# Performance work log

Measured on AMD Instinct MI355X. Metric: run time of the kernel, lower is better.

## Reference

```python
import jax, jax.numpy as jnp
import numpy as np
from jax import lax

# dims
N, CIN, COUT, CI, T, V = 128, 64, 64, 16, 128, 25
SS, ST = 3, 2  # num_subset_S, num_subset_T
BN_EPS = 1e-5
LRELU = 0.1


def _bn(x, p):
    # x: [N,C,T,V]; p: [4,C] = (gamma, beta, running_mean, running_var), eval-mode BN
    g, b, m, v = p
    inv = g / jnp.sqrt(v + BN_EPS)
    return (x - m[:, None, None]) * inv[:, None, None] + b[:, None, None]


def _c1x1(x, w, b):
    # 1x1 Conv2d: x [N,C,T,V], w [O,C], b [O]
    return jnp.einsum('nctv,oc->notv', x, w) + b[None, :, None, None]


def _lrelu(x):
    return jnp.where(x >= 0, x, LRELU * x)


def _bn_params(c):
    return jnp.stack([jnp.ones(c, jnp.float32), jnp.zeros(c, jnp.float32),
                      jnp.zeros(c, jnp.float32), jnp.ones(c, jnp.float32)])


def setup_inputs() -> dict:
    key = jax.random.key(0)
    ks = jax.random.split(key, 12)
    d = {}
    d['x'] = jax.random.normal(ks[0], (N, CIN, T, V), jnp.float32)
    # spatial attention projections
    d['w_in_s'] = jax.random.normal(ks[1], (2 * SS * CI, CIN), jnp.float32) * 0.1
    d['b_in_s'] = jnp.zeros((2 * SS * CI,), jnp.float32)
    d['alphas'] = jnp.ones((1, SS, 1, 1), jnp.float32)
    d['att0s'] = jnp.ones((1, SS, V, V), jnp.float32) / V
    d['w_out_s'] = jax.random.normal(ks[2], (COUT, SS * CIN), jnp.float32) * 0.05
    d['b_out_s'] = jnp.zeros((COUT,), jnp.float32)
    d['bn_out_s'] = _bn_params(COUT)
    d['w_ff_s'] = jax.random.normal(ks[3], (COUT, COUT), jnp.float32) * 0.1
    d['b_ff_s'] = jnp.zeros((COUT,), jnp.float32)
    d['bn_ff_s'] = _bn_params(COUT)
    # temporal attention projections (directed)
    d['w_in_t'] = jax.random.normal(ks[4], (4 * ST * CI, COUT), jnp.float32) * 0.1
    d['b_in_t'] = jnp.zeros((4 * ST * CI,), jnp.float32)
    d['alphat_f'] = jnp.ones((1, ST, 1, 1), jnp.float32)
    d['alphat_b'] = jnp.ones((1, ST, 1, 1), jnp.float32)
    d['w_out_t'] = jax.random.normal(ks[5], (COUT, 2 * ST * COUT), jnp.float32) * 0.05
    d['b_out_t'] = jnp.zeros((COUT,), jnp.float32)
    d['bn_out_t'] = _bn_params(COUT)
    d['w_ff_t'] = jax.random.normal(ks[6], (COUT, COUT), jnp.float32) * 0.1
    d['b_ff_t'] = jnp.zeros((COUT,), jnp.float32)
    d['bn_ff_t'] = _bn_params(COUT)
    # TCN extension (7x1 temporal conv)
    d['w_tcn'] = jax.random.normal(ks[7], (COUT, COUT, 7, 1), jnp.float32) * 0.03
    d['b_tcn'] = jnp.zeros((COUT,), jnp.float32)
    d['bn_tcn'] = _bn_params(COUT)
    return d


def _forward(x, w_in_s, b_in_s, alphas, att0s, w_out_s, b_out_s, bn_out_s,
             w_ff_s, b_ff_s, bn_ff_s, w_in_t, b_in_t, alphat_f, alphat_b,
             w_out_t, b_out_t, bn_out_t, w_ff_t, b_ff_t, bn_ff_t,
             w_tcn, b_tcn, bn_tcn):
    n, c, t, v = x.shape
    # ---- spatial attention ----
    qk = _c1x1(x, w_in_s, b_in_s).reshape(n, 2 * SS, CI, t, v)
    q, k = qk[:, :SS], qk[:, SS:]
    # atts buffer is zeros; attention = tanh(QK/(ci*T))*alpha + attention0s
    attn = jnp.tanh(jnp.einsum('nsctu,nsctv->nsuv', q, k) / (CI * t)) * alphas + att0s
    y = jnp.einsum('nctu,nsuv->nsctv', x, attn).reshape(n, SS * c, t, v)
    y = _bn(_c1x1(y, w_out_s, b_out_s), bn_out_s)
    y = _lrelu(x + y)            # downs1 = identity
    y2 = _bn(_c1x1(y, w_ff_s, b_ff_s), bn_ff_s)
    y = _lrelu(x + y2)           # downs2 = identity
    # ---- temporal attention (directed) ----
    qk = _c1x1(y, w_in_t, b_in_t).reshape(n, 4 * ST, CI, t, v)
    q_f, q_b = qk[:, :ST], qk[:, ST:2 * ST]
    k_f, k_b = qk[:, 2 * ST:3 * ST], qk[:, 3 * ST:]
    bmask = jnp.triu(jnp.ones((t, t), x.dtype))
    fmask = bmask.T
    a_b = jnp.tanh(jnp.einsum('nsctv,nscqv->nstq', q_b, k_b) / (CI * v)) * alphat_b * bmask
    a_f = jnp.tanh(jnp.einsum('nsctv,nscqv->nstq', q_f, k_f) / (CI * v)) * alphat_f * fmask
    z_f = jnp.einsum('nctv,nstq->nscqv', y, a_f).reshape(n, ST * COUT, t, v)
    z_b = jnp.einsum('nctv,nstq->nscqv', y, a_b).reshape(n, ST * COUT, t, v)
    z = jnp.concatenate([z_f, z_b], axis=1)
    z = _bn(_c1x1(z, w_out_t, b_out_t), bn_out_t)
    z = _lrelu(y + z)            # downt1 = identity
    z2 = _bn(_c1x1(z, w_ff_t, b_ff_t), bn_ff_t)
    z = _lrelu(y + z2)           # downt2 = identity
    # ---- TCN extension: residual 7x1 temporal conv, downt3 = identity ----
    tcn = lax.conv_general_dilated(z, w_tcn, (1, 1), ((3, 3), (0, 0)),
                                   dimension_numbers=('NCHW', 'OIHW', 'NCHW'))
    tcn = _bn(tcn + b_tcn[None, :, None, None], bn_tcn)
    z = _lrelu(z + tcn)
    return z


def reference(x, w_in_s, b_in_s, alphas, att0s, w_out_s, b_out_s, bn_out_s,
              w_ff_s, b_ff_s, bn_ff_s, w_in_t, b_in_t, alphat_f, alphat_b,
              w_out_t, b_out_t, bn_out_t, w_ff_t, b_ff_t, bn_ff_t,
              w_tcn, b_tcn, bn_tcn):
    return _forward(x, w_in_s, b_in_s, alphas, att0s, w_out_s, b_out_s, bn_out_s,
                    w_ff_s, b_ff_s, bn_ff_s, w_in_t, b_in_t, alphat_f, alphat_b,
                    w_out_t, b_out_t, bn_out_t, w_ff_t, b_ff_t, bn_ff_t,
                    w_tcn, b_tcn, bn_tcn)
```

## Files before the change

kernel.cpp:

```cpp
#include <hip/hip_runtime.h>
#include <math.h>

#define NN   128
#define TTc  128
#define VVc  25
#define TV   3200
#define BN_EPS 1e-5f

typedef __attribute__((ext_vector_type(8))) short bf8;
typedef __attribute__((ext_vector_type(4))) short s4;
typedef __attribute__((ext_vector_type(4))) float f4;

#define MFMA(a,b,c) __builtin_amdgcn_mfma_f32_16x16x32_bf16(a,b,c,0,0,0)

__device__ __forceinline__ float lrelu(float a){ return a>=0.f ? a : 0.1f*a; }
__device__ __forceinline__ short f2bs(float f){
    union{float f; unsigned u;} x; x.f = f;
    unsigned r = x.u + 0x7FFF + ((x.u>>16)&1);
    return (short)(r>>16);
}
__device__ __forceinline__ float b2f(short s){
    union{unsigned u; float f;} x; x.u = ((unsigned)(unsigned short)s)<<16; return x.f;
}
__device__ __forceinline__ s4 packf4(float a,float b,float c,float d){
    s4 r; r.x=f2bs(a); r.y=f2bs(b); r.z=f2bs(c); r.w=f2bs(d); return r;
}


__global__ __launch_bounds__(256) void k_prep(
    const float* __restrict__ w_in_s, const float* __restrict__ w_out_s,
    const float* __restrict__ w_ff_s, const float* __restrict__ w_in_t,
    const float* __restrict__ w_out_t, const float* __restrict__ w_ff_t,
    const float* __restrict__ w_tcn, short* __restrict__ wb)
{
    const int total = 51200 + 64*448;
    for (int i = blockIdx.x*256 + threadIdx.x; i < total; i += gridDim.x*256) {
        float v;
        if      (i < 6144)  v = w_in_s[i];
        else if (i < 18432) v = w_out_s[i-6144];
        else if (i < 22528) v = w_ff_s[i-18432];
        else if (i < 30720) v = w_in_t[i-22528];
        else if (i < 47104) v = w_out_t[i-30720];
        else if (i < 51200) v = w_ff_t[i-47104];
        else { int j=i-51200; int o=j/448; int r=j%448; int dt=r>>6; int c=r&63;
               v = w_tcn[(o*64+c)*7 + dt]; }
        wb[i] = f2bs(v);
    }
}

__global__ __launch_bounds__(256) void k_x2b(const float* __restrict__ x, short* __restrict__ XB)
{
    const int n = blockIdx.x >> 4, tc = blockIdx.x & 15, t0 = tc*8;
    const int tid = threadIdx.x;
    __shared__ float xs[64][203];
    const float* xb = x + (size_t)n*204800 + t0*25;
    for (int i = tid; i < 64*200; i += 256) { int c=i/200, p=i%200; xs[c][p] = xb[(size_t)c*3200 + p]; }
    __syncthreads();
    short* ob = XB + (size_t)n*204800 + t0*25*64;
    for (int i = tid; i < 200*16; i += 256) {
        const int p = i>>4, c0 = (i&15)<<2;
        *(s4*)&ob[p*64 + c0] = packf4(xs[c0][p], xs[c0+1][p], xs[c0+2][p], xs[c0+3][p]);
    }
}

__global__ __launch_bounds__(256) void k_attn_s(
    const short* __restrict__ XB, const short* __restrict__ wb,
    const float* __restrict__ b_in_s, const float* __restrict__ alphas,
    const float* __restrict__ att0s, short* __restrict__ attnB)
{
    const int n = blockIdx.x / 3, s = blockIdx.x % 3;
    const int tid = threadIdx.x, w = tid>>6, lane = tid&63, lr = lane&15, lq = lane>>4;
    __shared__ short ys[208][72];
    __shared__ short qkl[208][40];
    __shared__ short wsl[32][72];
    __shared__ float bl[32];

    for (int i = tid; i < 32*8; i += 256) {
        const int cl = i>>3, seg = i&7;
        const int row = (cl < 16) ? (s*16 + cl) : (48 + s*16 + (cl-16));
        *(bf8*)&wsl[cl][seg*8] = *(const bf8*)&wb[row*64 + seg*8];
    }
    if (tid < 32) {
        const int row = (tid < 16) ? (s*16 + tid) : (48 + s*16 + (tid-16));
        bl[tid] = b_in_s[row];
    }

    const int mt = w>>1, sn = w&1;
    f4 acc = {0.f,0.f,0.f,0.f};

    for (int ch = 0; ch < 16; ++ch) {
        __syncthreads();
        for (int i = tid; i < 208*8; i += 256) {
            const int row = i>>3, seg = i&7;
            bf8 val = {0,0,0,0,0,0,0,0};
            if (row < 200)
                val = *(const bf8*)&XB[((size_t)n*3200 + ch*200 + row)*64 + seg*8];
            *(bf8*)&ys[row][seg*8] = val;
        }
        __syncthreads();
        for (int nn = 0; nn < 4; ++nn) {
            const int nt2 = w + nn*4;
            if (nt2 >= 13) break;
            const bf8 b0 = *(const bf8*)&ys[nt2*16+lr][lq*8];
            const bf8 b1 = *(const bf8*)&ys[nt2*16+lr][32+lq*8];
            for (int mt2 = 0; mt2 < 2; ++mt2) {
                f4 pa = {0.f,0.f,0.f,0.f};
                const bf8 a0 = *(const bf8*)&wsl[mt2*16+lr][lq*8];
                const bf8 a1 = *(const bf8*)&wsl[mt2*16+lr][32+lq*8];
                pa = MFMA(a0,b0,pa); pa = MFMA(a1,b1,pa);
                const int px = nt2*16+lr, c0 = mt2*16+lq*4;
                *(s4*)&qkl[px][c0] =
                    packf4(pa.x+bl[c0], pa.y+bl[c0+1], pa.z+bl[c0+2], pa.w+bl[c0+3]);
            }
        }
        __syncthreads();
        for (int ks = 0; ks < 4; ++ks) {
            const int tl = ks*2 + (lq>>1);
            const bf8 af = *(const bf8*)&qkl[tl*25 + mt*16+lr][(lq&1)*8];
            const bf8 bf = *(const bf8*)&qkl[tl*25 + sn*16+lr][16 + (lq&1)*8];
            acc = MFMA(af, bf, acc);
        }
    }
    const float alpha = alphas[s];
    const int v = sn*16 + lr, u0 = mt*16 + lq*4;
    float r[4];
    #pragma unroll
    for (int j = 0; j < 4; ++j) {
        const int u = u0 + j;
        const float a = (j==0)?acc.x:((j==1)?acc.y:((j==2)?acc.z:acc.w));
        r[j] = (u < 25 && v < 25)
             ? tanhf(a*(1.f/2048.f))*alpha + att0s[s*625 + u*25 + v] : 0.f;
    }
    *(s4*)&attnB[(size_t)n*3072 + v*96 + s*32 + u0] = packf4(r[0],r[1],r[2],r[3]);
}

__global__ __launch_bounds__(256) void k_spatial(
    const short* __restrict__ XB, const short* __restrict__ attnB, const short* __restrict__ wb,
    const float* __restrict__ b_out, const float* __restrict__ bn_out,
    const float* __restrict__ b_ff,  const float* __restrict__ bn_ff,
    short* __restrict__ Y)
{
    const int n = blockIdx.x >> 5, tc = blockIdx.x & 31, t0 = tc*4;
    const int tid = threadIdx.x;
    const int w = tid>>6, lane = tid&63, lr = lane&15, lq = lane>>4;
    __shared__ short xs[4][32][72];
    __shared__ short wlo[64][200];
    __shared__ short wlf[64][72];
    __shared__ short ab[32][104];
    __shared__ short gsT[4][64][104];
    __shared__ short y1[4][32][72];
    __shared__ float sc1s[64], sh1s[64], sc2s[64], sh2s[64];

    for (int i = tid; i < 4*32*8; i += 256) {
        const int row = i>>3, seg = i&7, tl = row>>5, uv = row&31;
        bf8 val = {0,0,0,0,0,0,0,0};
        if (uv < 25) val = *(const bf8*)&XB[((size_t)n*3200 + (t0+tl)*25 + uv)*64 + seg*8];
        *(bf8*)&xs[tl][uv][seg*8] = val;
    }
    for (int i = tid; i < 64*24; i += 256) {
        const int o = i/24, seg = i%24;
        *(bf8*)&wlo[o][seg*8] = *(const bf8*)&wb[6144 + o*192 + seg*8];
    }
    for (int i = tid; i < 64*8; i += 256) {
        const int o = i>>3, seg = i&7;
        *(bf8*)&wlf[o][seg*8] = *(const bf8*)&wb[18432 + o*64 + seg*8];
    }
    for (int i = tid; i < 32*12; i += 256) {
        const int v = i/12, seg = i%12;
        *(bf8*)&ab[v][seg*8] = *(const bf8*)&attnB[(size_t)n*3072 + v*96 + seg*8];
    }
    if (tid < 64) {
        float g=bn_out[tid], bb=bn_out[64+tid], m=bn_out[128+tid], vv=bn_out[192+tid];
        float inv = g*rsqrtf(vv+BN_EPS);
        sc1s[tid]=inv; sh1s[tid]=(b_out[tid]-m)*inv+bb;
        g=bn_ff[tid]; bb=bn_ff[64+tid]; m=bn_ff[128+tid]; vv=bn_ff[192+tid];
        inv = g*rsqrtf(vv+BN_EPS);
        sc2s[tid]=inv; sh2s[tid]=(b_ff[tid]-m)*inv+bb;
    }
    __syncthreads();

    const int t = t0 + w;
    for (int s = 0; s < 3; ++s) {
        for (int mt = 0; mt < 2; ++mt) {
            const bf8 a0 = *(const bf8*)&xs[w][mt*16+lr][lq*8];
            const bf8 a1 = *(const bf8*)&xs[w][mt*16+lr][32+lq*8];
            for (int nt = 0; nt < 4; ++nt) {
                f4 acc = {0.f,0.f,0.f,0.f};
                const bf8 b0 = *(const bf8*)&wlo[nt*16+lr][s*64 + lq*8];
                const bf8 b1 = *(const bf8*)&wlo[nt*16+lr][s*64 + 32 + lq*8];
                acc = MFMA(a0,b0,acc); acc = MFMA(a1,b1,acc);
                const int o = nt*16+lr, u0 = mt*16+lq*4;
                *(s4*)&gsT[w][o][s*32+u0] = packf4(acc.x,acc.y,acc.z,acc.w);
            }
        }
    }
    for (int mt = 0; mt < 4; ++mt) {
        const bf8 a0 = *(const bf8*)&gsT[w][mt*16+lr][lq*8];
        const bf8 a1 = *(const bf8*)&gsT[w][mt*16+lr][32+lq*8];
        const bf8 a2 = *(const bf8*)&gsT[w][mt*16+lr][64+lq*8];
        for (int nt = 0; nt < 2; ++nt) {
            f4 acc = {0.f,0.f,0.f,0.f};
            const bf8 b0 = *(const bf8*)&ab[nt*16+lr][lq*8];
            const bf8 b1 = *(const bf8*)&ab[nt*16+lr][32+lq*8];
            const bf8 b2 = *(const bf8*)&ab[nt*16+lr][64+lq*8];
            acc = MFMA(a0,b0,acc); acc = MFMA(a1,b1,acc); acc = MFMA(a2,b2,acc);
            const int v = nt*16+lr, o0 = mt*16+lq*4;
            const s4 xr = *(const s4*)&xs[w][v][o0];
            const float r0 = lrelu(acc.x*sc1s[o0  ]+sh1s[o0  ]+b2f(xr.x));
            const float r1 = lrelu(acc.y*sc1s[o0+1]+sh1s[o0+1]+b2f(xr.y));
            const float r2 = lrelu(acc.z*sc1s[o0+2]+sh1s[o0+2]+b2f(xr.z));
            const float r3 = lrelu(acc.w*sc1s[o0+3]+sh1s[o0+3]+b2f(xr.w));
            *(s4*)&y1[w][v][o0] = packf4(r0,r1,r2,r3);
        }
    }
    for (int mt = 0; mt < 4; ++mt) {
        const bf8 a0 = *(const bf8*)&wlf[mt*16+lr][lq*8];
        const bf8 a1 = *(const bf8*)&wlf[mt*16+lr][32+lq*8];
        for (int nt = 0; nt < 2; ++nt) {
            f4 acc = {0.f,0.f,0.f,0.f};
            const bf8 b0 = *(const bf8*)&y1[w][nt*16+lr][lq*8];
            const bf8 b1 = *(const bf8*)&y1[w][nt*16+lr][32+lq*8];
            acc = MFMA(a0,b0,acc); acc = MFMA(a1,b1,acc);
            const int v = nt*16+lr, o0 = mt*16+lq*4;
            if (v < 25) {
                const s4 xr = *(const s4*)&xs[w][v][o0];
                const float r0 = lrelu(acc.x*sc2s[o0  ]+sh2s[o0  ]+b2f(xr.x));
                const float r1 = lrelu(acc.y*sc2s[o0+1]+sh2s[o0+1]+b2f(xr.y));
                const float r2 = lrelu(acc.z*sc2s[o0+2]+sh2s[o0+2]+b2f(xr.z));
                const float r3 = lrelu(acc.w*sc2s[o0+3]+sh2s[o0+3]+b2f(xr.w));
                *(s4*)&Y[((size_t)n*3200 + t*25 + v)*64 + o0] = packf4(r0,r1,r2,r3);
            }
        }
    }
}

__global__ __launch_bounds__(256) void k_qkt(
    const short* __restrict__ Y, const short* __restrict__ wb,
    const float* __restrict__ b_in_t, short* __restrict__ qkt)
{
    const int n = blockIdx.x >> 5, tc = blockIdx.x & 31, t0 = tc*4;
    const int tid = threadIdx.x;
    const int w = tid>>6, lane = tid&63, lr = lane&15, lq = lane>>4;
    __shared__ short ys[4][32][72];
    __shared__ short wi[128][72];
    for (int i = tid; i < 4*32*8; i += 256) {
        const int row = i>>3, seg = i&7, tl = row>>5, v = row&31;
        bf8 val = {0,0,0,0,0,0,0,0};
        if (v < 25) val = *(const bf8*)&Y[((size_t)n*3200 + (t0+tl)*25 + v)*64 + seg*8];
        *(bf8*)&ys[tl][v][seg*8] = val;
    }
    for (int i = tid; i < 128*8; i += 256) {
        const int o = i>>3, seg = i&7;
        *(bf8*)&wi[o][seg*8] = *(const bf8*)&wb[22528 + o*64 + seg*8];
    }
    __syncthreads();
    for (int mi = 0; mi < 2; ++mi) {
        const int mt = w*2+mi, tl = mt>>1, vh = mt&1;
        const bf8 a0 = *(const bf8*)&ys[tl][vh*16+lr][lq*8];
        const bf8 a1 = *(const bf8*)&ys[tl][vh*16+lr][32+lq*8];
        for (int nt = 0; nt < 8; ++nt) {
            f4 acc = {0.f,0.f,0.f,0.f};
            const bf8 b0 = *(const bf8*)&wi[nt*16+lr][lq*8];
            const bf8 b1 = *(const bf8*)&wi[nt*16+lr][32+lq*8];
            acc = MFMA(a0,b0,acc); acc = MFMA(a1,b1,acc);
            const int oc = nt*16+lr, v0 = vh*16+lq*4, t = t0+tl;
            const float bias = b_in_t[oc];
            const size_t base = (size_t)n*409600 + (size_t)t*3200 + oc*25 + v0;
            if (v0 < 24)
                *(s4*)&qkt[base] = packf4(acc.x+bias, acc.y+bias, acc.z+bias, acc.w+bias);
            else if (v0 == 24)
                qkt[base] = f2bs(acc.x+bias);
        }
    }
}

__global__ __launch_bounds__(256) void k_score_t(
    const short* __restrict__ qkt, const float* __restrict__ alphat_f,
    const float* __restrict__ alphat_b, short* __restrict__ aT)
{
    const int n = blockIdx.x >> 2, ds = blockIdx.x & 3, dir = ds>>1, s = ds&1;
    const int qoff = dir*32 + s*16, koff = 64 + dir*32 + s*16;
    const float alpha = dir ? alphat_b[s] : alphat_f[s];
    const int tid = threadIdx.x, w = tid>>6, lane = tid&63, lr = lane&15, lq = lane>>4;
    const short* qb = qkt + (size_t)n*409600;
    short* ao = aT + (size_t)(n*4+ds)*16384;
    const bf8 zf = {0,0,0,0,0,0,0,0};
    for (int ni = 0; ni < 2; ++ni) {
        const int nt = w*2+ni;
        for (int mt = 0; mt < 8; ++mt) {
            const int q = nt*16+lr, t0r = mt*16+lq*4;
            const bool skip = (dir==0) ? (mt < nt) : (mt > nt);
            if (skip) { s4 z = {0,0,0,0}; *(s4*)&ao[q*128 + t0r] = z; continue; }
            f4 acc = {0.f,0.f,0.f,0.f};
            for (int ks = 0; ks < 13; ++ks) {
                bf8 af, bf;
                if (ks==12 && lq>=2) { af = zf; bf = zf; }
                else {
                    af = *(const bf8*)&qb[(size_t)(mt*16+lr)*3200 + qoff*25 + ks*32 + lq*8];
                    bf = *(const bf8*)&qb[(size_t)(nt*16+lr)*3200 + koff*25 + ks*32 + lq*8];
                }
                acc = MFMA(af, bf, acc);
            }
            float r[4];
            #pragma unroll
            for (int j = 0; j < 4; ++j) {
                const int tt = t0r + j;
                const bool ok = (dir==0) ? (tt >= q) : (tt <= q);
                const float a = (j==0)?acc.x:((j==1)?acc.y:((j==2)?acc.z:acc.w));
                r[j] = ok ? tanhf(a*(1.f/400.f))*alpha : 0.f;
            }
            *(s4*)&ao[q*128 + t0r] = packf4(r[0],r[1],r[2],r[3]);
        }
    }
}

__global__ __launch_bounds__(256, 3) void k_tagg(
    const short* __restrict__ Y, const short* __restrict__ wb,
    const short* __restrict__ aT, short* __restrict__ U)
{
    const int n = blockIdx.x / 25, v = blockIdx.x % 25;
    const int tid = threadIdx.x, w = tid>>6, lane = tid&63, lr = lane&15, lq = lane>>4;
    __shared__ short ys[128][72];
    __shared__ short pt[2][64][136];

    for (int i = tid; i < 128*8; i += 256) {
        const int t = i>>3, seg = i&7;
        *(bf8*)&ys[t][seg*8] = *(const bf8*)&Y[((size_t)n*3200 + t*25 + v)*64 + seg*8];
    }
    bf8 wr[4][2];
    #pragma unroll
    for (int ds = 0; ds < 4; ++ds) {
        wr[ds][0] = *(const bf8*)&wb[30720 + (w*16+lr)*256 + ds*64 + lq*8];
        wr[ds][1] = *(const bf8*)&wb[30720 + (w*16+lr)*256 + ds*64 + 32 + lq*8];
    }

    f4 acc[2][4];
    #pragma unroll
    for (int mi = 0; mi < 2; ++mi)
        #pragma unroll
        for (int nt = 0; nt < 4; ++nt) { acc[mi][nt].x=0.f; acc[mi][nt].y=0.f; acc[mi][nt].z=0.f; acc[mi][nt].w=0.f; }

    __syncthreads();

    #pragma unroll
    for (int ds = 0; ds < 4; ++ds) {
        const int dir = ds>>1, buf = ds&1;
        bf8 ar[2][4];
        #pragma unroll
        for (int mi = 0; mi < 2; ++mi) {
            const int qt = 2*w + mi;
            #pragma unroll
            for (int ks = 0; ks < 4; ++ks) {
                const bool skip = (dir==0) ? (ks*32+31 < qt*16) : (ks*32 > qt*16+15);
                if (!skip)
                    ar[mi][ks] = *(const bf8*)&aT[(size_t)(n*4+ds)*16384
                                                  + (qt*16+lr)*128 + ks*32 + lq*8];
            }
        }
        {
            const bf8 b0 = wr[ds][0], b1 = wr[ds][1];
            #pragma unroll
            for (int tt = 0; tt < 8; ++tt) {
                f4 p = {0.f,0.f,0.f,0.f};
                const bf8 a0 = *(const bf8*)&ys[tt*16+lr][lq*8];
                const bf8 a1 = *(const bf8*)&ys[tt*16+lr][32+lq*8];
                p = MFMA(a0,b0,p); p = MFMA(a1,b1,p);
                *(s4*)&pt[buf][w*16+lr][tt*16+lq*4] = packf4(p.x,p.y,p.z,p.w);
            }
        }
        __syncthreads();
        #pragma unroll
        for (int ks = 0; ks < 4; ++ks) {
            const bool skip0 = (dir==0) ? (ks*32+31 < (2*w)*16)   : (ks*32 > (2*w)*16+15);
            const bool skip1 = (dir==0) ? (ks*32+31 < (2*w+1)*16) : (ks*32 > (2*w+1)*16+15);
            if (skip0 && skip1) continue;
            bf8 bfr[4];
            #pragma unroll
            for (int nt = 0; nt < 4; ++nt)
                bfr[nt] = *(const bf8*)&pt[buf][nt*16+lr][ks*32+lq*8];
            if (!skip0) {
                #pragma unroll
                for (int nt = 0; nt < 4; ++nt)
                    acc[0][nt] = MFMA(ar[0][ks], bfr[nt], acc[0][nt]);
            }
            if (!skip1) {
                #pragma unroll
                for (int nt = 0; nt < 4; ++nt)
                    acc[1][nt] = MFMA(ar[1][ks], bfr[nt], acc[1][nt]);
            }
        }
    }
    #pragma unroll
    for (int mi = 0; mi < 2; ++mi) {
        #pragma unroll
        for (int j = 0; j < 4; ++j) {
            const int q = (2*w+mi)*16 + lq*4 + j;
            short* ub = &U[((size_t)(n*128+q)*25 + v)*64 + lr];
            ub[0]  = f2bs(acc[mi][0][j]);
            ub[16] = f2bs(acc[mi][1][j]);
            ub[32] = f2bs(acc[mi][2][j]);
            ub[48] = f2bs(acc[mi][3][j]);
        }
    }
}

__global__ __launch_bounds__(256) void k_temporal(
    const short* __restrict__ U, short* __restrict__ Y, const short* __restrict__ wb,
    const float* __restrict__ b_out, const float* __restrict__ bn_out,
    const float* __restrict__ b_ff,  const float* __restrict__ bn_ff)
{
    const int n = blockIdx.x >> 5, qc = blockIdx.x & 31, q0 = qc*4;
    const int tid = threadIdx.x, w = tid>>6, lane = tid&63, lr = lane&15, lq = lane>>4;
    __shared__ short zs[112][72];
    __shared__ short z1[112][72];
    __shared__ short zout[112][72];
    __shared__ short wf[64][72];
    __shared__ float sc1s[64], sh1s[64], sc2s[64], sh2s[64];
    if (tid < 64) {
        float g=bn_out[tid], bb=bn_out[64+tid], m=bn_out[128+tid], vv=bn_out[192+tid];
        float inv = g*rsqrtf(vv+BN_EPS);
        sc1s[tid]=inv; sh1s[tid]=(b_out[tid]-m)*inv+bb;
        g=bn_ff[tid]; bb=bn_ff[64+tid]; m=bn_ff[128+tid]; vv=bn_ff[192+tid];
        inv = g*rsqrtf(vv+BN_EPS);
        sc2s[tid]=inv; sh2s[tid]=(b_ff[tid]-m)*inv+bb;
    }
    for (int i = tid; i < 64*8; i += 256) {
        const int o = i>>3, seg = i&7;
        *(bf8*)&wf[o][seg*8] = *(const bf8*)&wb[47104 + o*64 + seg*8];
    }
    __syncthreads();
    for (int i = tid; i < 112*8; i += 256) {
        const int row = i>>3, seg = i&7;
        bf8 yv = {0,0,0,0,0,0,0,0}, zv = yv;
        if (row < 100) {
            const int q = q0 + row/25, v = row%25;
            yv = *(const bf8*)&Y[((size_t)n*3200 + q*25 + v)*64 + seg*8];
            const bf8 uv = *(const bf8*)&U[((size_t)(n*128+q)*25 + v)*64 + seg*8];
            #pragma unroll
            for (int j = 0; j < 8; ++j) {
                const int o = seg*8+j;
                zv[j] = f2bs(lrelu(b2f(yv[j]) + b2f(uv[j])*sc1s[o] + sh1s[o]));
            }
        }
        *(bf8*)&zs[row][seg*8] = yv;
        *(bf8*)&z1[row][seg*8] = zv;
    }
    __syncthreads();
    const bf8 a0 = *(const bf8*)&wf[w*16+lr][lq*8];
    const bf8 a1 = *(const bf8*)&wf[w*16+lr][32+lq*8];
    for (int nt = 0; nt < 7; ++nt) {
        f4 acc = {0.f,0.f,0.f,0.f};
        const bf8 b0 = *(const bf8*)&z1[nt*16+lr][lq*8];
        const bf8 b1 = *(const bf8*)&z1[nt*16+lr][32+lq*8];
        acc = MFMA(a0,b0,acc); acc = MFMA(a1,b1,acc);
        const int px = nt*16+lr, o0 = w*16+lq*4;
        const s4 yr = *(const s4*)&zs[px][o0];
        const float r0 = lrelu(acc.x*sc2s[o0  ]+sh2s[o0  ]+b2f(yr.x));
        const float r1 = lrelu(acc.y*sc2s[o0+1]+sh2s[o0+1]+b2f(yr.y));
        const float r2 = lrelu(acc.z*sc2s[o0+2]+sh2s[o0+2]+b2f(yr.z));
        const float r3 = lrelu(acc.w*sc2s[o0+3]+sh2s[o0+3]+b2f(yr.w));
        *(s4*)&zout[px][o0] = packf4(r0,r1,r2,r3);
    }
    __syncthreads();
    for (int i = tid; i < 100*8; i += 256) {
        const int row = i>>3, seg = i&7;
        *(bf8*)&Y[((size_t)n*3200 + q0*25 + row)*64 + seg*8] = *(const bf8*)&zout[row][seg*8];
    }
}

__global__ __launch_bounds__(256, 2) void k_tcn(
    const short* __restrict__ Y, const short* __restrict__ wb,
    const float* __restrict__ b, const float* __restrict__ bn,
    float* __restrict__ out)
{
    const int n = blockIdx.x >> 5, tc = (blockIdx.x >> 1) & 15, oh = blockIdx.x & 1;
    const int t0 = tc*8;
    const int tid = threadIdx.x, w = tid>>6, lane = tid&63, lr = lane&15, lq = lane>>4;
    __shared__ short zs[352][72];
    __shared__ float scs[32], shs[32];

    bf8 af[2][14];
    #pragma unroll
    for (int mt = 0; mt < 2; ++mt)
        #pragma unroll
        for (int st = 0; st < 14; ++st)
            af[mt][st] = *(const bf8*)&wb[51200 + (oh*32 + mt*16 + lr)*448 + st*32 + lq*8];

    if (tid < 32) {
        const int o = oh*32 + tid;
        const float g=bn[o], bb=bn[64+o], m=bn[128+o], vv=bn[192+o];
        const float inv = g*rsqrtf(vv+BN_EPS);
        scs[tid]=inv; shs[tid]=(b[o]-m)*inv+bb;
    }
    for (int i = tid; i < 352*8; i += 256) {
        const int row = i>>3, seg = i&7;
        bf8 val = {0,0,0,0,0,0,0,0};
        if (row < 350) {
            const int tlp = row/25, v = row%25, t = t0 - 3 + tlp;
            if (t >= 0 && t < 128)
                val = *(const bf8*)&Y[((size_t)n*3200 + t*25 + v)*64 + seg*8];
        }
        *(bf8*)&zs[row][seg*8] = val;
    }
    __syncthreads();
    for (int nn = 0; nn < 4; ++nn) {
        const int nt = w + nn*4;
        if (nt >= 13) break;
        bf8 bfr[14];
        #pragma unroll
        for (int st = 0; st < 14; ++st)
            bfr[st] = *(const bf8*)&zs[nt*16 + lr + (st>>1)*25][(st&1)*32 + lq*8];
        f4 ac[2][4];
        #pragma unroll
        for (int m2 = 0; m2 < 2; ++m2)
            #pragma unroll
            for (int j = 0; j < 4; ++j) { ac[m2][j].x=0.f; ac[m2][j].y=0.f; ac[m2][j].z=0.f; ac[m2][j].w=0.f; }
        #pragma unroll
        for (int st = 0; st < 14; ++st) {
            ac[0][st&3] = MFMA(af[0][st], bfr[st], ac[0][st&3]);
            ac[1][st&3] = MFMA(af[1][st], bfr[st], ac[1][st&3]);
        }
        const int px = nt*16+lr;
        if (px < 200) {
            #pragma unroll
            for (int mt = 0; mt < 2; ++mt) {
                const float ax = ac[mt][0].x+ac[mt][1].x+ac[mt][2].x+ac[mt][3].x;
                const float ay = ac[mt][0].y+ac[mt][1].y+ac[mt][2].y+ac[mt][3].y;
                const float az = ac[mt][0].z+ac[mt][1].z+ac[mt][2].z+ac[mt][3].z;
                const float aw = ac[mt][0].w+ac[mt][1].w+ac[mt][2].w+ac[mt][3].w;
                const int o0l = mt*16+lq*4;
                const s4 zr = *(const s4*)&zs[px+75][oh*32+o0l];
                float* ob = out + (size_t)n*204800 + (size_t)(oh*32+o0l)*3200 + t0*25 + px;
                ob[0]    = lrelu(ax*scs[o0l  ]+shs[o0l  ]+b2f(zr.x));
                ob[3200] = lrelu(ay*scs[o0l+1]+shs[o0l+1]+b2f(zr.y));
                ob[6400] = lrelu(az*scs[o0l+2]+shs[o0l+2]+b2f(zr.z));
                ob[9600] = lrelu(aw*scs[o0l+3]+shs[o0l+3]+b2f(zr.w));
            }
        }
    }
}

extern "C" void kernel_launch(void* const* d_in, const int* in_sizes, int n_in,
                              void* d_out, int out_size, void* d_ws, size_t ws_size,
                              hipStream_t stream) {
    const float* x        = (const float*)d_in[0];
    const float* w_in_s   = (const float*)d_in[1];
    const float* b_in_s   = (const float*)d_in[2];
    const float* alphas   = (const float*)d_in[3];
    const float* att0s    = (const float*)d_in[4];
    const float* w_out_s  = (const float*)d_in[5];
    const float* b_out_s  = (const float*)d_in[6];
    const float* bn_out_s = (const float*)d_in[7];
    const float* w_ff_s   = (const float*)d_in[8];
    const float* b_ff_s   = (const float*)d_in[9];
    const float* bn_ff_s  = (const float*)d_in[10];
    const float* w_in_t   = (const float*)d_in[11];
    const float* b_in_t   = (const float*)d_in[12];
    const float* alphat_f = (const float*)d_in[13];
    const float* alphat_b = (const float*)d_in[14];
    const float* w_out_t  = (const float*)d_in[15];
    const float* b_out_t  = (const float*)d_in[16];
    const float* bn_out_t = (const float*)d_in[17];
    const float* w_ff_t   = (const float*)d_in[18];
    const float* b_ff_t   = (const float*)d_in[19];
    const float* bn_ff_t  = (const float*)d_in[20];
    const float* w_tcn    = (const float*)d_in[21];
    const float* b_tcn    = (const float*)d_in[22];
    const float* bn_tcn   = (const float*)d_in[23];
    float* out = (float*)d_out;
    char* ws = (char*)d_ws;

    short* wb    = (short*)(ws + 0);
    short* attnB = (short*)(ws + 4102144);
    short* Y     = (short*)(ws + 4888576);
    short* aT    = (short*)(ws + 57317376);
    short* XB    = (short*)(ws + 74094592);
    short* QKT   = (short*)(ws + 74094592);
    short* U     = (short*)(ws + 74094592 + 52428800);

    k_prep<<<64, 256, 0, stream>>>(w_in_s, w_out_s, w_ff_s, w_in_t, w_out_t, w_ff_t, w_tcn, wb);
    k_x2b<<<2048, 256, 0, stream>>>(x, XB);
    k_attn_s<<<NN * 3, 256, 0, stream>>>(XB, wb, b_in_s, alphas, att0s, attnB);
    k_spatial<<<4096, 256, 0, stream>>>(XB, attnB, wb, b_out_s, bn_out_s, b_ff_s, bn_ff_s, Y);
    k_qkt<<<4096, 256, 0, stream>>>(Y, wb, b_in_t, QKT);
    k_score_t<<<512, 256, 0, stream>>>(QKT, alphat_f, alphat_b, aT);
    k_tagg<<<NN * 25, 256, 0, stream>>>(Y, wb, aT, U);
    k_temporal<<<4096, 256, 0, stream>>>(U, Y, wb, b_out_t, bn_out_t, b_ff_t, bn_ff_t);
    k_tcn<<<4096, 256, 0, stream>>>(Y, wb, b_tcn, bn_tcn, out);
}
```

Before: 714.7 us.

## Keep spatial-kernel weights and attention fragments in registers, shrink LDS use

Rewrites k_spatial so the out-projection, feed-forward weights and attention operands are loaded straight from global memory into register fragments instead of being staged in shared memory. The per-subset intermediate now goes into a smaller LDS buffer, with the attention MFMA accumulated per subset. This cuts LDS footprint and staging work, and launch_bounds(256,2) is requested to raise occupancy. The cost is more register pressure and repeated global (cache) loads of the weights by every wave.

```diff
diff --git a/kernel.cpp b/kernel.cpp
--- a/kernel.cpp
+++ b/kernel.cpp
@@ -134,7 +134,7 @@
     *(s4*)&attnB[(size_t)n*3072 + v*96 + s*32 + u0] = packf4(r[0],r[1],r[2],r[3]);
 }
 
-__global__ __launch_bounds__(256) void k_spatial(
+__global__ __launch_bounds__(256, 2) void k_spatial(
     const short* __restrict__ XB, const short* __restrict__ attnB, const short* __restrict__ wb,
     const float* __restrict__ b_out, const float* __restrict__ bn_out,
     const float* __restrict__ b_ff,  const float* __restrict__ bn_ff,
@@ -144,30 +144,28 @@
     const int tid = threadIdx.x;
     const int w = tid>>6, lane = tid&63, lr = lane&15, lq = lane>>4;
     __shared__ short xs[4][32][72];
-    __shared__ short wlo[64][200];
-    __shared__ short wlf[64][72];
-    __shared__ short ab[32][104];
-    __shared__ short gsT[4][64][104];
+    __shared__ short gst[4][64][40];
     __shared__ short y1[4][32][72];
     __shared__ float sc1s[64], sh1s[64], sc2s[64], sh2s[64];
+
+    bf8 abf[2][3];
+    #pragma unroll
+    for (int nt = 0; nt < 2; ++nt)
+        #pragma unroll
+        for (int s = 0; s < 3; ++s)
+            abf[nt][s] = *(const bf8*)&attnB[(size_t)n*3072 + (nt*16+lr)*96 + s*32 + lq*8];
+    bf8 wff[4][2];
+    #pragma unroll
+    for (int mt = 0; mt < 4; ++mt) {
+        wff[mt][0] = *(const bf8*)&wb[18432 + (mt*16+lr)*64 + lq*8];
+        wff[mt][1] = *(const bf8*)&wb[18432 + (mt*16+lr)*64 + 32 + lq*8];
+    }
 
     for (int i = tid; i < 4*32*8; i += 256) {
         const int row = i>>3, seg = i&7, tl = row>>5, uv = row&31;
         bf8 val = {0,0,0,0,0,0,0,0};
         if (uv < 25) val = *(const bf8*)&XB[((size_t)n*3200 + (t0+tl)*25 + uv)*64 + seg*8];
         *(bf8*)&xs[tl][uv][seg*8] = val;
-    }
-    for (int i = tid; i < 64*24; i += 256) {
-        const int o = i/24, seg = i%24;
-        *(bf8*)&wlo[o][seg*8] = *(const bf8*)&wb[6144 + o*192 + seg*8];
-    }
-    for (int i = tid; i < 64*8; i += 256) {
-        const int o = i>>3, seg = i&7;
-        *(bf8*)&wlf[o][seg*8] = *(const bf8*)&wb[18432 + o*64 + seg*8];
-    }
-    for (int i = tid; i < 32*12; i += 256) {
-        const int v = i/12, seg = i%12;
-        *(bf8*)&ab[v][seg*8] = *(const bf8*)&attnB[(size_t)n*3072 + v*96 + seg*8];
     }
     if (tid < 64) {
         float g=bn_out[tid], bb=bn_out[64+tid], m=bn_out[128+tid], vv=bn_out[192+tid];
@@ -179,32 +177,48 @@
     }
     __syncthreads();
 
-    const int t = t0 + w;
+    f4 acc2[4][2];
+    #pragma unroll
+    for (int mt = 0; mt < 4; ++mt)
+        #pragma unroll
+        for (int nt = 0; nt < 2; ++nt) { acc2[mt][nt].x=0.f; acc2[mt][nt].y=0.f; acc2[mt][nt].z=0.f; acc2[mt][nt].w=0.f; }
+
+    #pragma unroll
     for (int s = 0; s < 3; ++s) {
+        bf8 wof[4][2];
+        #pragma unroll
+        for (int nt = 0; nt < 4; ++nt) {
+            wof[nt][0] = *(const bf8*)&wb[6144 + (nt*16+lr)*192 + s*64 + lq*8];
+            wof[nt][1] = *(const bf8*)&wb[6144 + (nt*16+lr)*192 + s*64 + 32 + lq*8];
+        }
+        #pragma unroll
         for (int mt = 0; mt < 2; ++mt) {
             const bf8 a0 = *(const bf8*)&xs[w][mt*16+lr][lq*8];
             const bf8 a1 = *(const bf8*)&xs[w][mt*16+lr][32+lq*8];
+            #pragma unroll
             for (int nt = 0; nt < 4; ++nt) {
                 f4 acc = {0.f,0.f,0.f,0.f};
-                const bf8 b0 = *(const bf8*)&wlo[nt*16+lr][s*64 + lq*8];
-                const bf8 b1 = *(const bf8*)&wlo[nt*16+lr][s*64 + 32 + lq*8];
-                acc = MFMA(a0,b0,acc); acc = MFMA(a1,b1,acc);
-                const int o = nt*16+lr, u0 = mt*16+lq*4;
-                *(s4*)&gsT[w][o][s*32+u0] = packf4(acc.x,acc.y,acc.z,acc.w);
-            }
-        }
-    }
+                acc = MFMA(a0, wof[nt][0], acc);
+                acc = MFMA(a1, wof[nt][1], acc);
+                *(s4*)&gst[w][nt*16+lr][mt*16+lq*4] = packf4(acc.x,acc.y,acc.z,acc.w);
+            }
+        }
+        #pragma unroll
+        for (int mt = 0; mt < 4; ++mt) {
+            const bf8 a = *(const bf8*)&gst[w][mt*16+lr][lq*8];
+            #pragma unroll
+            for (int nt = 0; nt < 2; ++nt)
+                acc2[mt][nt] = MFMA(a, abf[nt][s], acc2[mt][nt]);
+        }
+    }
+
+    const int t = t0 + w;
+    #pragma unroll
     for (int mt = 0; mt < 4; ++mt) {
-        const bf8 a0 = *(const bf8*)&gsT[w][mt*16+lr][lq*8];
-        const bf8 a1 = *(const bf8*)&gsT[w][mt*16+lr][32+lq*8];
-        const bf8 a2 = *(const bf8*)&gsT[w][mt*16+lr][64+lq*8];
+        #pragma unroll
         for (int nt = 0; nt < 2; ++nt) {
-            f4 acc = {0.f,0.f,0.f,0.f};
-            const bf8 b0 = *(const bf8*)&ab[nt*16+lr][lq*8];
-            const bf8 b1 = *(const bf8*)&ab[nt*16+lr][32+lq*8];
-            const bf8 b2 = *(const bf8*)&ab[nt*16+lr][64+lq*8];
-            acc = MFMA(a0,b0,acc); acc = MFMA(a1,b1,acc); acc = MFMA(a2,b2,acc);
             const int v = nt*16+lr, o0 = mt*16+lq*4;
+            const f4 acc = acc2[mt][nt];
             const s4 xr = *(const s4*)&xs[w][v][o0];
             const float r0 = lrelu(acc.x*sc1s[o0  ]+sh1s[o0  ]+b2f(xr.x));
             const float r1 = lrelu(acc.y*sc1s[o0+1]+sh1s[o0+1]+b2f(xr.y));
@@ -213,14 +227,14 @@
             *(s4*)&y1[w][v][o0] = packf4(r0,r1,r2,r3);
         }
     }
+    #pragma unroll
     for (int mt = 0; mt < 4; ++mt) {
-        const bf8 a0 = *(const bf8*)&wlf[mt*16+lr][lq*8];
-        const bf8 a1 = *(const bf8*)&wlf[mt*16+lr][32+lq*8];
+        #pragma unroll
         for (int nt = 0; nt < 2; ++nt) {
             f4 acc = {0.f,0.f,0.f,0.f};
             const bf8 b0 = *(const bf8*)&y1[w][nt*16+lr][lq*8];
             const bf8 b1 = *(const bf8*)&y1[w][nt*16+lr][32+lq*8];
-            acc = MFMA(a0,b0,acc); acc = MFMA(a1,b1,acc);
+            acc = MFMA(wff[mt][0],b0,acc); acc = MFMA(wff[mt][1],b1,acc);
             const int v = nt*16+lr, o0 = mt*16+lq*4;
             if (v < 25) {
                 const s4 xr = *(const s4*)&xs[w][v][o0];
```

After: 691.0 us. -3.3%, faster.
